# Optimization experiments

Measured on AMD Instinct MI355X. Metric: run time of the kernel, lower is better.

## Reference

```python
import jax, jax.numpy as jnp
import numpy as np

V_SRC, V_DST = 32000, 32000
E, H = 512, 512
B, S = 64, 2048


def setup_inputs() -> dict:
    key = jax.random.key(0)
    ks = jax.random.split(key, 12)
    sc = 0.02  # weight init scale
    return {
        "dec_inputs": jax.random.randint(ks[0], (1, B), 0, V_SRC, dtype=jnp.int64 if jax.config.jax_enable_x64 else jnp.int32),
        "enc_outputs": jax.random.normal(ks[1], (S, B, H), jnp.float32),
        "h0": jax.random.normal(ks[2], (1, B, H), jnp.float32),
        "emb": jax.random.normal(ks[3], (V_SRC, E), jnp.float32) * sc,
        "W_ih": jax.random.normal(ks[4], (3 * H, E), jnp.float32) * sc,
        "W_hh": jax.random.normal(ks[5], (3 * H, H), jnp.float32) * sc,
        "b_ih": jax.random.normal(ks[6], (3 * H,), jnp.float32) * sc,
        "b_hh": jax.random.normal(ks[7], (3 * H,), jnp.float32) * sc,
        "W_attn": jax.random.normal(ks[8], (H, H), jnp.float32) * sc,
        "b_attn": jax.random.normal(ks[9], (H,), jnp.float32) * sc,
        "W_cls": jax.random.normal(ks[10], (V_DST, 2 * H), jnp.float32) * sc,
        "b_cls": jax.random.normal(ks[11], (V_DST,), jnp.float32) * sc,
    }


def _gru_step(x, h, W_ih, W_hh, b_ih, b_hh):
    # x: [B, E], h: [B, H]  (PyTorch GRU gate layout: r, z, n)
    gi = x @ W_ih.T + b_ih          # [B, 3H]
    gh = h @ W_hh.T + b_hh          # [B, 3H]
    hdim = h.shape[-1]
    r = jax.nn.sigmoid(gi[:, :hdim] + gh[:, :hdim])
    z = jax.nn.sigmoid(gi[:, hdim:2 * hdim] + gh[:, hdim:2 * hdim])
    n = jnp.tanh(gi[:, 2 * hdim:] + r * gh[:, 2 * hdim:])
    return (1.0 - z) * n + z * h


def reference(dec_inputs, enc_outputs, h0, emb, W_ih, W_hh, b_ih, b_hh,
              W_attn, b_attn, W_cls, b_cls):
    # embedding + ReLU, single decode step
    x = jax.nn.relu(emb[dec_inputs[0]])                    # [B, E]
    h = _gru_step(x, h0[0], W_ih, W_hh, b_ih, b_hh)        # [B, H] == dec_output.squeeze(0)
    dec_hidden = h[None]                                   # [1, B, H]

    # attention: vectorized form of the per-timestep loop
    e = enc_outputs @ W_attn.T + b_attn                    # [S, B, H]
    alpha = jnp.einsum('sbh,bh->bs', e, h)                 # [B, S]
    scores = jax.nn.softmax(alpha, axis=1)                 # [B, S]
    context = jnp.einsum('bs,sbh->bh', scores, enc_outputs)  # [B, H]

    logits = jnp.concatenate([h, context], axis=1) @ W_cls.T + b_cls  # [B, V_dst]
    out = jax.nn.log_softmax(logits, axis=1)
    return (out, dec_hidden)
```

## Files before the change

kernel.cpp:

```cpp
#include <hip/hip_runtime.h>
#include <hip/hip_bf16.h>
#include <math.h>

#define V_SRC 32000
#define V_DST 32000
#define EDIM  512
#define HDIM  512
#define BB    64
#define SS    2048
#define G3H   1536

__global__ __launch_bounds__(128) void k_embed(const int* __restrict__ idx,
                                               const float* __restrict__ emb,
                                               float* __restrict__ x) {
    int b = blockIdx.x;
    int t = threadIdx.x;
    int row = idx[b];
    float4 v = *(const float4*)(emb + (size_t)row * EDIM + t * 4);
    v.x = fmaxf(v.x, 0.f); v.y = fmaxf(v.y, 0.f);
    v.z = fmaxf(v.z, 0.f); v.w = fmaxf(v.w, 0.f);
    *(float4*)(x + (size_t)b * EDIM + t * 4) = v;
}

__global__ __launch_bounds__(256) void k_gru_gemv(const float* __restrict__ x,
                                                  const float* __restrict__ h0,
                                                  const float* __restrict__ W_ih,
                                                  const float* __restrict__ W_hh,
                                                  float* __restrict__ gi,
                                                  float* __restrict__ gh) {
    int w    = threadIdx.x >> 6;
    int lane = threadIdx.x & 63;
    int j    = blockIdx.x * 4 + w;

    float4 wi1 = *(const float4*)(W_ih + (size_t)j * EDIM + lane * 4);
    float4 wi2 = *(const float4*)(W_ih + (size_t)j * EDIM + 256 + lane * 4);
    float4 wh1 = *(const float4*)(W_hh + (size_t)j * HDIM + lane * 4);
    float4 wh2 = *(const float4*)(W_hh + (size_t)j * HDIM + 256 + lane * 4);

    for (int b = 0; b < BB; b++) {
        float4 x1 = *(const float4*)(x  + (size_t)b * EDIM + lane * 4);
        float4 x2 = *(const float4*)(x  + (size_t)b * EDIM + 256 + lane * 4);
        float4 h1 = *(const float4*)(h0 + (size_t)b * HDIM + lane * 4);
        float4 h2 = *(const float4*)(h0 + (size_t)b * HDIM + 256 + lane * 4);
        float pi = x1.x*wi1.x + x1.y*wi1.y + x1.z*wi1.z + x1.w*wi1.w
                 + x2.x*wi2.x + x2.y*wi2.y + x2.z*wi2.z + x2.w*wi2.w;
        float ph = h1.x*wh1.x + h1.y*wh1.y + h1.z*wh1.z + h1.w*wh1.w
                 + h2.x*wh2.x + h2.y*wh2.y + h2.z*wh2.z + h2.w*wh2.w;
        #pragma unroll
        for (int off = 32; off; off >>= 1) {
            pi += __shfl_xor(pi, off);
            ph += __shfl_xor(ph, off);
        }
        if (lane == 0) {
            gi[(size_t)b * G3H + j] = pi;
            gh[(size_t)b * G3H + j] = ph;
        }
    }
}

__device__ __forceinline__ float sigmoidf_(float v) {
    return 1.f / (1.f + __expf(-v));
}

__global__ __launch_bounds__(128) void k_gru_gates(const float* __restrict__ gi,
                                                   const float* __restrict__ gh,
                                                   const float* __restrict__ h0,
                                                   const float* __restrict__ b_ih,
                                                   const float* __restrict__ b_hh,
                                                   float* __restrict__ concat,
                                                   float* __restrict__ hout) {
    int b = blockIdx.x;
    int i = threadIdx.x * 4;
    const float* gib = gi + (size_t)b * G3H;
    const float* ghb = gh + (size_t)b * G3H;

    float4 gir = *(const float4*)(gib + i);
    float4 giz = *(const float4*)(gib + i + 512);
    float4 gin = *(const float4*)(gib + i + 1024);
    float4 ghr = *(const float4*)(ghb + i);
    float4 ghz = *(const float4*)(ghb + i + 512);
    float4 ghn = *(const float4*)(ghb + i + 1024);
    float4 bir = *(const float4*)(b_ih + i);
    float4 biz = *(const float4*)(b_ih + i + 512);
    float4 bin = *(const float4*)(b_ih + i + 1024);
    float4 bhr = *(const float4*)(b_hh + i);
    float4 bhz = *(const float4*)(b_hh + i + 512);
    float4 bhn = *(const float4*)(b_hh + i + 1024);
    float4 hv  = *(const float4*)(h0 + (size_t)b * HDIM + i);

    float4 o;
    {
        float r = sigmoidf_(gir.x + bir.x + ghr.x + bhr.x);
        float z = sigmoidf_(giz.x + biz.x + ghz.x + bhz.x);
        float n = tanhf(gin.x + bin.x + r * (ghn.x + bhn.x));
        o.x = (1.f - z) * n + z * hv.x;
    }
    {
        float r = sigmoidf_(gir.y + bir.y + ghr.y + bhr.y);
        float z = sigmoidf_(giz.y + biz.y + ghz.y + bhz.y);
        float n = tanhf(gin.y + bin.y + r * (ghn.y + bhn.y));
        o.y = (1.f - z) * n + z * hv.y;
    }
    {
        float r = sigmoidf_(gir.z + bir.z + ghr.z + bhr.z);
        float z = sigmoidf_(giz.z + biz.z + ghz.z + bhz.z);
        float n = tanhf(gin.z + bin.z + r * (ghn.z + bhn.z));
        o.z = (1.f - z) * n + z * hv.z;
    }
    {
        float r = sigmoidf_(gir.w + bir.w + ghr.w + bhr.w);
        float z = sigmoidf_(giz.w + biz.w + ghz.w + bhz.w);
        float n = tanhf(gin.w + bin.w + r * (ghn.w + bhn.w));
        o.w = (1.f - z) * n + z * hv.w;
    }
    *(float4*)(concat + (size_t)b * 1024 + i) = o;
    *(float4*)(hout   + (size_t)b * HDIM + i) = o;
}

__global__ __launch_bounds__(256) void k_attn_u(const float* __restrict__ concat,
                                                const float* __restrict__ W_attn,
                                                float* __restrict__ u) {
    int b = blockIdx.x;
    int j = threadIdx.x;
    const float* hrow = concat + (size_t)b * 1024;
    float a0 = 0.f, a1 = 0.f;
    for (int i = 0; i < HDIM; i++) {
        float hvv = hrow[i];
        a0 = fmaf(hvv, W_attn[(size_t)i * HDIM + j],       a0);
        a1 = fmaf(hvv, W_attn[(size_t)i * HDIM + j + 256], a1);
    }
    u[(size_t)b * HDIM + j]       = a0;
    u[(size_t)b * HDIM + j + 256] = a1;
}

__global__ __launch_bounds__(256) void k_attn_flash(const float* __restrict__ enc,
                                                    const float* __restrict__ u,
                                                    float* __restrict__ pm,
                                                    float* __restrict__ pl,
                                                    float* __restrict__ pacc) {
    int tile = blockIdx.x;
    int b    = blockIdx.y;
    int w    = threadIdx.x >> 6;
    int lane = threadIdx.x & 63;

    float4 u1 = *(const float4*)(u + (size_t)b * HDIM + lane * 4);
    float4 u2 = *(const float4*)(u + (size_t)b * HDIM + 256 + lane * 4);

    float m = -INFINITY, l = 0.f;
    float4 a1 = {0.f, 0.f, 0.f, 0.f};
    float4 a2 = {0.f, 0.f, 0.f, 0.f};

    for (int it = 0; it < 16; it++) {
        int s = tile * 64 + it * 4 + w;
        const float* row = enc + ((size_t)s * BB + b) * HDIM;
        float4 e1 = *(const float4*)(row + lane * 4);
        float4 e2 = *(const float4*)(row + 256 + lane * 4);
        float p = e1.x*u1.x + e1.y*u1.y + e1.z*u1.z + e1.w*u1.w
                + e2.x*u2.x + e2.y*u2.y + e2.z*u2.z + e2.w*u2.w;
        #pragma unroll
        for (int off = 32; off; off >>= 1) p += __shfl_xor(p, off);

        float wt;
        if (p > m) {
            float sc = __expf(m - p);
            l *= sc;
            a1.x *= sc; a1.y *= sc; a1.z *= sc; a1.w *= sc;
            a2.x *= sc; a2.y *= sc; a2.z *= sc; a2.w *= sc;
            m = p;
            wt = 1.f;
        } else {
            wt = __expf(p - m);
        }
        l += wt;
        a1.x = fmaf(wt, e1.x, a1.x); a1.y = fmaf(wt, e1.y, a1.y);
        a1.z = fmaf(wt, e1.z, a1.z); a1.w = fmaf(wt, e1.w, a1.w);
        a2.x = fmaf(wt, e2.x, a2.x); a2.y = fmaf(wt, e2.y, a2.y);
        a2.z = fmaf(wt, e2.z, a2.z); a2.w = fmaf(wt, e2.w, a2.w);
    }

    __shared__ float sm[4], sl[4];
    __shared__ float sacc[4][512];
    if (lane == 0) { sm[w] = m; sl[w] = l; }
    *(float4*)&sacc[w][lane * 4]       = a1;
    *(float4*)&sacc[w][256 + lane * 4] = a2;
    __syncthreads();

    float M  = fmaxf(fmaxf(sm[0], sm[1]), fmaxf(sm[2], sm[3]));
    float s0 = __expf(sm[0] - M), s1 = __expf(sm[1] - M);
    float s2 = __expf(sm[2] - M), s3 = __expf(sm[3] - M);
    float L  = s0 * sl[0] + s1 * sl[1] + s2 * sl[2] + s3 * sl[3];

    int tid  = threadIdx.x;
    int pidx = b * 32 + tile;
    float acc0 = s0 * sacc[0][tid] + s1 * sacc[1][tid]
               + s2 * sacc[2][tid] + s3 * sacc[3][tid];
    float acc1 = s0 * sacc[0][tid + 256] + s1 * sacc[1][tid + 256]
               + s2 * sacc[2][tid + 256] + s3 * sacc[3][tid + 256];
    if (tid == 0) { pm[pidx] = M; pl[pidx] = L; }
    pacc[(size_t)pidx * HDIM + tid]       = acc0;
    pacc[(size_t)pidx * HDIM + tid + 256] = acc1;
}

__global__ __launch_bounds__(256) void k_attn_combine(const float* __restrict__ pm,
                                                      const float* __restrict__ pl,
                                                      const float* __restrict__ pacc,
                                                      float* __restrict__ concat) {
    int b   = blockIdx.x;
    int tid = threadIdx.x;
    __shared__ float smv[32], spl[32], ssc[32];
    if (tid < 32) {
        smv[tid] = pm[b * 32 + tid];
        spl[tid] = pl[b * 32 + tid];
    }
    __syncthreads();
    float M = smv[0];
    #pragma unroll
    for (int t = 1; t < 32; t++) M = fmaxf(M, smv[t]);
    if (tid < 32) ssc[tid] = __expf(smv[tid] - M);
    __syncthreads();

    float L = 0.f;
    #pragma unroll
    for (int t = 0; t < 32; t++) L += ssc[t] * spl[t];

    float c0 = 0.f, c1 = 0.f;
    for (int t = 0; t < 32; t++) {
        const float* pa = pacc + (size_t)(b * 32 + t) * HDIM;
        c0 = fmaf(ssc[t], pa[tid],       c0);
        c1 = fmaf(ssc[t], pa[tid + 256], c1);
    }
    float inv = 1.f / L;
    concat[(size_t)b * 1024 + 512 + tid]       = c0 * inv;
    concat[(size_t)b * 1024 + 512 + tid + 256] = c1 * inv;
}

#define LDSTR 68

__global__ __launch_bounds__(256) void k_classifier(const float* __restrict__ concat,
                                                    const float* __restrict__ W_cls,
                                                    const float* __restrict__ b_cls,
                                                    float* __restrict__ logits) {
    __shared__ float A_lds[64 * LDSTR];
    __shared__ float W_lds[64 * LDSTR];
    int t  = threadIdx.x;
    int tx = t & 15;
    int ty = t >> 4;
    int vbase = blockIdx.x * 64;
    int swz = (tx & 7) << 2;

    float acc[4][4] = {};

    for (int kc = 0; kc < 16; kc++) {
        int k0 = kc * 64;
        #pragma unroll
        for (int j = 0; j < 4; j++) {
            int idx = t + j * 256;
            int row = idx >> 4;
            int col = (idx & 15) * 4;
            float4 av = *(const float4*)(concat + (size_t)row * 1024 + k0 + col);
            *(float4*)&A_lds[row * LDSTR + col] = av;
            float4 wv = *(const float4*)(W_cls + (size_t)(vbase + row) * 1024 + k0 + col);
            int csw = col ^ (((row >> 2) & 7) << 2);
            *(float4*)&W_lds[row * LDSTR + csw] = wv;
        }
        __syncthreads();

        #pragma unroll
        for (int ks = 0; ks < 16; ks++) {
            int kk = ks * 4;
            int kw = kk ^ swz;
            float4 a0 = *(float4*)&A_lds[(ty * 4 + 0) * LDSTR + kk];
            float4 a1 = *(float4*)&A_lds[(ty * 4 + 1) * LDSTR + kk];
            float4 a2 = *(float4*)&A_lds[(ty * 4 + 2) * LDSTR + kk];
            float4 a3 = *(float4*)&A_lds[(ty * 4 + 3) * LDSTR + kk];
            float4 w0 = *(float4*)&W_lds[(tx * 4 + 0) * LDSTR + kw];
            float4 w1 = *(float4*)&W_lds[(tx * 4 + 1) * LDSTR + kw];
            float4 w2 = *(float4*)&W_lds[(tx * 4 + 2) * LDSTR + kw];
            float4 w3 = *(float4*)&W_lds[(tx * 4 + 3) * LDSTR + kw];
            float4 aa[4] = {a0, a1, a2, a3};
            float4 ww[4] = {w0, w1, w2, w3};
            #pragma unroll
            for (int i = 0; i < 4; i++)
                #pragma unroll
                for (int jj = 0; jj < 4; jj++) {
                    acc[i][jj] = fmaf(aa[i].x, ww[jj].x, acc[i][jj]);
                    acc[i][jj] = fmaf(aa[i].y, ww[jj].y, acc[i][jj]);
                    acc[i][jj] = fmaf(aa[i].z, ww[jj].z, acc[i][jj]);
                    acc[i][jj] = fmaf(aa[i].w, ww[jj].w, acc[i][jj]);
                }
        }
        __syncthreads();
    }

    float4 bc = *(const float4*)(b_cls + vbase + tx * 4);
    #pragma unroll
    for (int i = 0; i < 4; i++) {
        float4 o;
        o.x = acc[i][0] + bc.x;
        o.y = acc[i][1] + bc.y;
        o.z = acc[i][2] + bc.z;
        o.w = acc[i][3] + bc.w;
        *(float4*)&logits[(size_t)(ty * 4 + i) * V_DST + vbase + tx * 4] = o;
    }
}

__global__ __launch_bounds__(256) void k_logsoftmax(float* __restrict__ logits) {
    int b    = blockIdx.x;
    int tid  = threadIdx.x;
    int w    = tid >> 6, lane = tid & 63;
    float4* row = (float4*)(logits + (size_t)b * V_DST);
    __shared__ float sm4[4], sl4[4];

    float m = -INFINITY;
    for (int i = tid; i < 8000; i += 256) {
        float4 v = row[i];
        m = fmaxf(m, fmaxf(fmaxf(v.x, v.y), fmaxf(v.z, v.w)));
    }
    #pragma unroll
    for (int off = 32; off; off >>= 1) m = fmaxf(m, __shfl_xor(m, off));
    if (lane == 0) sm4[w] = m;
    __syncthreads();
    float M = fmaxf(fmaxf(sm4[0], sm4[1]), fmaxf(sm4[2], sm4[3]));

    float l = 0.f;
    for (int i = tid; i < 8000; i += 256) {
        float4 v = row[i];
        l += __expf(v.x - M) + __expf(v.y - M) + __expf(v.z - M) + __expf(v.w - M);
    }
    #pragma unroll
    for (int off = 32; off; off >>= 1) l += __shfl_xor(l, off);
    if (lane == 0) sl4[w] = l;
    __syncthreads();
    float L   = sl4[0] + sl4[1] + sl4[2] + sl4[3];
    float lse = M + logf(L);

    for (int i = tid; i < 8000; i += 256) {
        float4 v = row[i];
        v.x -= lse; v.y -= lse; v.z -= lse; v.w -= lse;
        row[i] = v;
    }
}

extern "C" void kernel_launch(void* const* d_in, const int* in_sizes, int n_in,
                              void* d_out, int out_size, void* d_ws, size_t ws_size,
                              hipStream_t stream) {
    const int*   dec_inputs = (const int*)  d_in[0];
    const float* enc        = (const float*)d_in[1];
    const float* h0         = (const float*)d_in[2];
    const float* emb        = (const float*)d_in[3];
    const float* W_ih       = (const float*)d_in[4];
    const float* W_hh       = (const float*)d_in[5];
    const float* b_ih       = (const float*)d_in[6];
    const float* b_hh       = (const float*)d_in[7];
    const float* W_attn     = (const float*)d_in[8];
    const float* W_cls      = (const float*)d_in[10];
    const float* b_cls      = (const float*)d_in[11];

    float* out  = (float*)d_out;
    float* hout = out + (size_t)BB * V_DST;

    float* ws     = (float*)d_ws;
    float* x      = ws;
    float* gi     = ws + 32768;
    float* gh     = ws + 131072;
    float* concat = ws + 229376;
    float* u      = ws + 294912;
    float* pm     = ws + 327680;
    float* pl     = ws + 329728;
    float* pacc   = ws + 331776;

    k_embed      <<<64,          128, 0, stream>>>(dec_inputs, emb, x);
    k_gru_gemv   <<<384,         256, 0, stream>>>(x, h0, W_ih, W_hh, gi, gh);
    k_gru_gates  <<<64,          128, 0, stream>>>(gi, gh, h0, b_ih, b_hh, concat, hout);
    k_attn_u     <<<64,          256, 0, stream>>>(concat, W_attn, u);
    k_attn_flash <<<dim3(32,64), 256, 0, stream>>>(enc, u, pm, pl, pacc);
    k_attn_combine<<<64,         256, 0, stream>>>(pm, pl, pacc, concat);
    k_classifier <<<500,         256, 0, stream>>>(concat, W_cls, b_cls, out);
    k_logsoftmax <<<64,          256, 0, stream>>>(out);
}
```

Before: 641.7 us.

## Use split-bf16 MFMA classifier, fuse embed into GRU, split attention projection, partial log-softmax

The classifier GEMM now runs on bf16 MFMA instructions. Activations are pre-split into high and low bf16 halves and weights are split on the fly, with three MFMA products per step to approximate fp32 accuracy. The classifier also emits per-block max and sum partials, so the log-softmax kernel only needs one read-modify-write pass instead of three passes over the logits. The embedding gather with ReLU is fused into the GRU GEMV, and the attention projection is split over K chunks for more parallelism. The three-term bf16 split may lose some precision compared with fp32 FMA.

```diff
diff --git a/kernel.cpp b/kernel.cpp
--- a/kernel.cpp
+++ b/kernel.cpp
@@ -10,19 +10,25 @@
 #define SS    2048
 #define G3H   1536
 
-__global__ __launch_bounds__(128) void k_embed(const int* __restrict__ idx,
-                                               const float* __restrict__ emb,
-                                               float* __restrict__ x) {
-    int b = blockIdx.x;
-    int t = threadIdx.x;
-    int row = idx[b];
-    float4 v = *(const float4*)(emb + (size_t)row * EDIM + t * 4);
-    v.x = fmaxf(v.x, 0.f); v.y = fmaxf(v.y, 0.f);
-    v.z = fmaxf(v.z, 0.f); v.w = fmaxf(v.w, 0.f);
-    *(float4*)(x + (size_t)b * EDIM + t * 4) = v;
-}
-
-__global__ __launch_bounds__(256) void k_gru_gemv(const float* __restrict__ x,
+typedef __attribute__((ext_vector_type(8))) short bfrag8;
+typedef __attribute__((ext_vector_type(4))) float f4v;
+
+__device__ __forceinline__ void split_bf16(float x, unsigned short& h, unsigned short& l) {
+    unsigned u  = __float_as_uint(x);
+    unsigned hb = u & 0xFFFF0000u;
+    h = (unsigned short)(u >> 16);
+    float r = x - __uint_as_float(hb);
+    unsigned v = __float_as_uint(r);
+    v += 0x7FFFu + ((v >> 16) & 1u);
+    l = (unsigned short)(v >> 16);
+}
+
+__device__ __forceinline__ float sigmoidf_(float v) {
+    return 1.f / (1.f + __expf(-v));
+}
+
+__global__ __launch_bounds__(256) void k_gru_gemv(const int* __restrict__ idx,
+                                                  const float* __restrict__ emb,
                                                   const float* __restrict__ h0,
                                                   const float* __restrict__ W_ih,
                                                   const float* __restrict__ W_hh,
@@ -38,8 +44,14 @@
     float4 wh2 = *(const float4*)(W_hh + (size_t)j * HDIM + 256 + lane * 4);
 
     for (int b = 0; b < BB; b++) {
-        float4 x1 = *(const float4*)(x  + (size_t)b * EDIM + lane * 4);
-        float4 x2 = *(const float4*)(x  + (size_t)b * EDIM + 256 + lane * 4);
+        int row = idx[b];
+        const float* er = emb + (size_t)row * EDIM;
+        float4 x1 = *(const float4*)(er + lane * 4);
+        float4 x2 = *(const float4*)(er + 256 + lane * 4);
+        x1.x = fmaxf(x1.x, 0.f); x1.y = fmaxf(x1.y, 0.f);
+        x1.z = fmaxf(x1.z, 0.f); x1.w = fmaxf(x1.w, 0.f);
+        x2.x = fmaxf(x2.x, 0.f); x2.y = fmaxf(x2.y, 0.f);
+        x2.z = fmaxf(x2.z, 0.f); x2.w = fmaxf(x2.w, 0.f);
         float4 h1 = *(const float4*)(h0 + (size_t)b * HDIM + lane * 4);
         float4 h2 = *(const float4*)(h0 + (size_t)b * HDIM + 256 + lane * 4);
         float pi = x1.x*wi1.x + x1.y*wi1.y + x1.z*wi1.z + x1.w*wi1.w
@@ -58,17 +70,15 @@
     }
 }
 
-__device__ __forceinline__ float sigmoidf_(float v) {
-    return 1.f / (1.f + __expf(-v));
-}
-
 __global__ __launch_bounds__(128) void k_gru_gates(const float* __restrict__ gi,
                                                    const float* __restrict__ gh,
                                                    const float* __restrict__ h0,
                                                    const float* __restrict__ b_ih,
                                                    const float* __restrict__ b_hh,
-                                                   float* __restrict__ concat,
-                                                   float* __restrict__ hout) {
+                                                   float* __restrict__ h,
+                                                   float* __restrict__ hout,
+                                                   unsigned short* __restrict__ cH,
+                                                   unsigned short* __restrict__ cL) {
     int b = blockIdx.x;
     int i = threadIdx.x * 4;
     const float* gib = gi + (size_t)b * G3H;
@@ -88,53 +98,55 @@
     float4 bhn = *(const float4*)(b_hh + i + 1024);
     float4 hv  = *(const float4*)(h0 + (size_t)b * HDIM + i);
 
-    float4 o;
-    {
-        float r = sigmoidf_(gir.x + bir.x + ghr.x + bhr.x);
-        float z = sigmoidf_(giz.x + biz.x + ghz.x + bhz.x);
-        float n = tanhf(gin.x + bin.x + r * (ghn.x + bhn.x));
-        o.x = (1.f - z) * n + z * hv.x;
-    }
-    {
-        float r = sigmoidf_(gir.y + bir.y + ghr.y + bhr.y);
-        float z = sigmoidf_(giz.y + biz.y + ghz.y + bhz.y);
-        float n = tanhf(gin.y + bin.y + r * (ghn.y + bhn.y));
-        o.y = (1.f - z) * n + z * hv.y;
-    }
-    {
-        float r = sigmoidf_(gir.z + bir.z + ghr.z + bhr.z);
-        float z = sigmoidf_(giz.z + biz.z + ghz.z + bhz.z);
-        float n = tanhf(gin.z + bin.z + r * (ghn.z + bhn.z));
-        o.z = (1.f - z) * n + z * hv.z;
-    }
-    {
-        float r = sigmoidf_(gir.w + bir.w + ghr.w + bhr.w);
-        float z = sigmoidf_(giz.w + biz.w + ghz.w + bhz.w);
-        float n = tanhf(gin.w + bin.w + r * (ghn.w + bhn.w));
-        o.w = (1.f - z) * n + z * hv.w;
-    }
-    *(float4*)(concat + (size_t)b * 1024 + i) = o;
-    *(float4*)(hout   + (size_t)b * HDIM + i) = o;
-}
-
-__global__ __launch_bounds__(256) void k_attn_u(const float* __restrict__ concat,
-                                                const float* __restrict__ W_attn,
-                                                float* __restrict__ u) {
-    int b = blockIdx.x;
-    int j = threadIdx.x;
-    const float* hrow = concat + (size_t)b * 1024;
+    float o[4], hvv[4] = {hv.x, hv.y, hv.z, hv.w};
+    float girv[4] = {gir.x, gir.y, gir.z, gir.w}, gizv[4] = {giz.x, giz.y, giz.z, giz.w};
+    float ginv[4] = {gin.x, gin.y, gin.z, gin.w}, ghrv[4] = {ghr.x, ghr.y, ghr.z, ghr.w};
+    float ghzv[4] = {ghz.x, ghz.y, ghz.z, ghz.w}, ghnv[4] = {ghn.x, ghn.y, ghn.z, ghn.w};
+    float birv[4] = {bir.x, bir.y, bir.z, bir.w}, bizv[4] = {biz.x, biz.y, biz.z, biz.w};
+    float binv[4] = {bin.x, bin.y, bin.z, bin.w}, bhrv[4] = {bhr.x, bhr.y, bhr.z, bhr.w};
+    float bhzv[4] = {bhz.x, bhz.y, bhz.z, bhz.w}, bhnv[4] = {bhn.x, bhn.y, bhn.z, bhn.w};
+
+    unsigned short hs[4], ls[4];
+    #pragma unroll
+    for (int q = 0; q < 4; q++) {
+        float r = sigmoidf_(girv[q] + birv[q] + ghrv[q] + bhrv[q]);
+        float z = sigmoidf_(gizv[q] + bizv[q] + ghzv[q] + bhzv[q]);
+        float n = tanhf(ginv[q] + binv[q] + r * (ghnv[q] + bhnv[q]));
+        o[q] = (1.f - z) * n + z * hvv[q];
+        split_bf16(o[q], hs[q], ls[q]);
+    }
+    float4 of = {o[0], o[1], o[2], o[3]};
+    *(float4*)(h    + (size_t)b * HDIM + i) = of;
+    *(float4*)(hout + (size_t)b * HDIM + i) = of;
+    ushort4 hh = {hs[0], hs[1], hs[2], hs[3]};
+    ushort4 ll = {ls[0], ls[1], ls[2], ls[3]};
+    *(ushort4*)(cH + (size_t)b * 1024 + i) = hh;
+    *(ushort4*)(cL + (size_t)b * 1024 + i) = ll;
+}
+
+__global__ __launch_bounds__(256) void k_u(const float* __restrict__ h,
+                                           const float* __restrict__ W_attn,
+                                           float* __restrict__ u_part) {
+    int kc = blockIdx.x;
+    int b  = blockIdx.y;
+    int t  = threadIdx.x;
+    __shared__ float hl[64];
+    if (t < 64) hl[t] = h[(size_t)b * HDIM + kc * 64 + t];
+    __syncthreads();
+    const float* Wp = W_attn + (size_t)(kc * 64) * HDIM;
     float a0 = 0.f, a1 = 0.f;
-    for (int i = 0; i < HDIM; i++) {
-        float hvv = hrow[i];
-        a0 = fmaf(hvv, W_attn[(size_t)i * HDIM + j],       a0);
-        a1 = fmaf(hvv, W_attn[(size_t)i * HDIM + j + 256], a1);
-    }
-    u[(size_t)b * HDIM + j]       = a0;
-    u[(size_t)b * HDIM + j + 256] = a1;
+    #pragma unroll 8
+    for (int i = 0; i < 64; i++) {
+        float hv = hl[i];
+        a0 = fmaf(hv, Wp[(size_t)i * HDIM + t],       a0);
+        a1 = fmaf(hv, Wp[(size_t)i * HDIM + t + 256], a1);
+    }
+    u_part[(size_t)(kc * 64 + b) * HDIM + t]       = a0;
+    u_part[(size_t)(kc * 64 + b) * HDIM + t + 256] = a1;
 }
 
 __global__ __launch_bounds__(256) void k_attn_flash(const float* __restrict__ enc,
-                                                    const float* __restrict__ u,
+                                                    const float* __restrict__ u_part,
                                                     float* __restrict__ pm,
                                                     float* __restrict__ pl,
                                                     float* __restrict__ pacc) {
@@ -143,8 +155,15 @@
     int w    = threadIdx.x >> 6;
     int lane = threadIdx.x & 63;
 
-    float4 u1 = *(const float4*)(u + (size_t)b * HDIM + lane * 4);
-    float4 u2 = *(const float4*)(u + (size_t)b * HDIM + 256 + lane * 4);
+    float4 u1 = {0.f,0.f,0.f,0.f}, u2 = {0.f,0.f,0.f,0.f};
+    #pragma unroll
+    for (int kc = 0; kc < 8; kc++) {
+        const float* up = u_part + (size_t)(kc * 64 + b) * HDIM;
+        float4 p1 = *(const float4*)(up + lane * 4);
+        float4 p2 = *(const float4*)(up + 256 + lane * 4);
+        u1.x += p1.x; u1.y += p1.y; u1.z += p1.z; u1.w += p1.w;
+        u2.x += p2.x; u2.y += p2.y; u2.z += p2.z; u2.w += p2.w;
+    }
 
     float m = -INFINITY, l = 0.f;
     float4 a1 = {0.f, 0.f, 0.f, 0.f};
@@ -204,7 +223,8 @@
 __global__ __launch_bounds__(256) void k_attn_combine(const float* __restrict__ pm,
                                                       const float* __restrict__ pl,
                                                       const float* __restrict__ pacc,
-                                                      float* __restrict__ concat) {
+                                                      unsigned short* __restrict__ cH,
+                                                      unsigned short* __restrict__ cL) {
     int b   = blockIdx.x;
     int tid = threadIdx.x;
     __shared__ float smv[32], spl[32], ssc[32];
@@ -230,111 +250,128 @@
         c1 = fmaf(ssc[t], pa[tid + 256], c1);
     }
     float inv = 1.f / L;
-    concat[(size_t)b * 1024 + 512 + tid]       = c0 * inv;
-    concat[(size_t)b * 1024 + 512 + tid + 256] = c1 * inv;
-}
-
-#define LDSTR 68
-
-__global__ __launch_bounds__(256) void k_classifier(const float* __restrict__ concat,
+    c0 *= inv; c1 *= inv;
+    unsigned short h0s, l0s, h1s, l1s;
+    split_bf16(c0, h0s, l0s);
+    split_bf16(c1, h1s, l1s);
+    cH[(size_t)b * 1024 + 512 + tid]       = h0s;
+    cL[(size_t)b * 1024 + 512 + tid]       = l0s;
+    cH[(size_t)b * 1024 + 512 + tid + 256] = h1s;
+    cL[(size_t)b * 1024 + 512 + tid + 256] = l1s;
+}
+
+__global__ __launch_bounds__(512) void k_classifier(const unsigned short* __restrict__ cH,
+                                                    const unsigned short* __restrict__ cL,
                                                     const float* __restrict__ W_cls,
                                                     const float* __restrict__ b_cls,
-                                                    float* __restrict__ logits) {
-    __shared__ float A_lds[64 * LDSTR];
-    __shared__ float W_lds[64 * LDSTR];
-    int t  = threadIdx.x;
-    int tx = t & 15;
-    int ty = t >> 4;
-    int vbase = blockIdx.x * 64;
-    int swz = (tx & 7) << 2;
-
-    float acc[4][4] = {};
-
-    for (int kc = 0; kc < 16; kc++) {
-        int k0 = kc * 64;
-        #pragma unroll
-        for (int j = 0; j < 4; j++) {
-            int idx = t + j * 256;
-            int row = idx >> 4;
-            int col = (idx & 15) * 4;
-            float4 av = *(const float4*)(concat + (size_t)row * 1024 + k0 + col);
-            *(float4*)&A_lds[row * LDSTR + col] = av;
-            float4 wv = *(const float4*)(W_cls + (size_t)(vbase + row) * 1024 + k0 + col);
-            int csw = col ^ (((row >> 2) & 7) << 2);
-            *(float4*)&W_lds[row * LDSTR + csw] = wv;
-        }
-        __syncthreads();
-
-        #pragma unroll
-        for (int ks = 0; ks < 16; ks++) {
-            int kk = ks * 4;
-            int kw = kk ^ swz;
-            float4 a0 = *(float4*)&A_lds[(ty * 4 + 0) * LDSTR + kk];
-            float4 a1 = *(float4*)&A_lds[(ty * 4 + 1) * LDSTR + kk];
-            float4 a2 = *(float4*)&A_lds[(ty * 4 + 2) * LDSTR + kk];
-            float4 a3 = *(float4*)&A_lds[(ty * 4 + 3) * LDSTR + kk];
-            float4 w0 = *(float4*)&W_lds[(tx * 4 + 0) * LDSTR + kw];
-            float4 w1 = *(float4*)&W_lds[(tx * 4 + 1) * LDSTR + kw];
-            float4 w2 = *(float4*)&W_lds[(tx * 4 + 2) * LDSTR + kw];
-            float4 w3 = *(float4*)&W_lds[(tx * 4 + 3) * LDSTR + kw];
-            float4 aa[4] = {a0, a1, a2, a3};
-            float4 ww[4] = {w0, w1, w2, w3};
-            #pragma unroll
-            for (int i = 0; i < 4; i++)
-                #pragma unroll
-                for (int jj = 0; jj < 4; jj++) {
-                    acc[i][jj] = fmaf(aa[i].x, ww[jj].x, acc[i][jj]);
-                    acc[i][jj] = fmaf(aa[i].y, ww[jj].y, acc[i][jj]);
-                    acc[i][jj] = fmaf(aa[i].z, ww[jj].z, acc[i][jj]);
-                    acc[i][jj] = fmaf(aa[i].w, ww[jj].w, acc[i][jj]);
-                }
-        }
-        __syncthreads();
-    }
-
-    float4 bc = *(const float4*)(b_cls + vbase + tx * 4);
-    #pragma unroll
-    for (int i = 0; i < 4; i++) {
-        float4 o;
-        o.x = acc[i][0] + bc.x;
-        o.y = acc[i][1] + bc.y;
-        o.z = acc[i][2] + bc.z;
-        o.w = acc[i][3] + bc.w;
-        *(float4*)&logits[(size_t)(ty * 4 + i) * V_DST + vbase + tx * 4] = o;
-    }
-}
-
-__global__ __launch_bounds__(256) void k_logsoftmax(float* __restrict__ logits) {
-    int b    = blockIdx.x;
-    int tid  = threadIdx.x;
-    int w    = tid >> 6, lane = tid & 63;
-    float4* row = (float4*)(logits + (size_t)b * V_DST);
+                                                    float* __restrict__ logits,
+                                                    float* __restrict__ pmax,
+                                                    float* __restrict__ psum) {
+    int t = threadIdx.x;
+    int w = t >> 6;
+    int l = t & 63;
+    int g = l >> 4;
+    int bl = l & 15;
+    int v_lane = blockIdx.x * 128 + w * 16 + bl;
+
+    const float* pW = W_cls + (size_t)v_lane * 1024 + g * 8;
+    const unsigned short* pAh[4];
+    const unsigned short* pAl[4];
+    #pragma unroll
+    for (int bq = 0; bq < 4; bq++) {
+        pAh[bq] = cH + (size_t)(bq * 16 + bl) * 1024 + g * 8;
+        pAl[bq] = cL + (size_t)(bq * 16 + bl) * 1024 + g * 8;
+    }
+
+    f4v acc[4] = {};
+
+    #pragma unroll 2
+    for (int k0 = 0; k0 < 1024; k0 += 32) {
+        float4 wf0 = *(const float4*)(pW + k0);
+        float4 wf1 = *(const float4*)(pW + k0 + 4);
+        float wf[8] = {wf0.x, wf0.y, wf0.z, wf0.w, wf1.x, wf1.y, wf1.z, wf1.w};
+        bfrag8 wh, wl;
+        #pragma unroll
+        for (int q = 0; q < 8; q++) {
+            unsigned short hs, ls;
+            split_bf16(wf[q], hs, ls);
+            wh[q] = (short)hs;
+            wl[q] = (short)ls;
+        }
+        #pragma unroll
+        for (int bq = 0; bq < 4; bq++) {
+            bfrag8 ah = *(const bfrag8*)(pAh[bq] + k0);
+            bfrag8 al = *(const bfrag8*)(pAl[bq] + k0);
+            acc[bq] = __builtin_amdgcn_mfma_f32_16x16x32_bf16(ah, wh, acc[bq], 0, 0, 0);
+            acc[bq] = __builtin_amdgcn_mfma_f32_16x16x32_bf16(al, wh, acc[bq], 0, 0, 0);
+            acc[bq] = __builtin_amdgcn_mfma_f32_16x16x32_bf16(ah, wl, acc[bq], 0, 0, 0);
+        }
+    }
+
+    float bias = b_cls[v_lane];
+
+    #pragma unroll
+    for (int bq = 0; bq < 4; bq++) {
+        #pragma unroll
+        for (int r = 0; r < 4; r++) {
+            float val = acc[bq][r] + bias;
+            int brow = bq * 16 + g * 4 + r;
+            logits[(size_t)brow * V_DST + v_lane] = val;
+        }
+    }
+    size_t pbase = ((size_t)blockIdx.x * 8 + w) * 64;
+    #pragma unroll
+    for (int bq = 0; bq < 4; bq++) {
+        #pragma unroll
+        for (int r = 0; r < 4; r++) {
+            float val = acc[bq][r] + bias;
+            float mv = val;
+            mv = fmaxf(mv, __shfl_xor(mv, 1));
+            mv = fmaxf(mv, __shfl_xor(mv, 2));
+            mv = fmaxf(mv, __shfl_xor(mv, 4));
+            mv = fmaxf(mv, __shfl_xor(mv, 8));
+            float e = __expf(val - mv);
+            e += __shfl_xor(e, 1);
+            e += __shfl_xor(e, 2);
+            e += __shfl_xor(e, 4);
+            e += __shfl_xor(e, 8);
+            if (bl == 0) {
+                int brow = bq * 16 + g * 4 + r;
+                pmax[pbase + brow] = mv;
+                psum[pbase + brow] = e;
+            }
+        }
+    }
+}
+
+__global__ __launch_bounds__(256) void k_lsm(const float* __restrict__ pmax,
+                                             const float* __restrict__ psum,
+                                             float* __restrict__ logits) {
+    int c = blockIdx.x;
+    int b = blockIdx.y;
+    int tid = threadIdx.x;
+    int w = tid >> 6, lane = tid & 63;
     __shared__ float sm4[4], sl4[4];
 
     float m = -INFINITY;
-    for (int i = tid; i < 8000; i += 256) {
-        float4 v = row[i];
-        m = fmaxf(m, fmaxf(fmaxf(v.x, v.y), fmaxf(v.z, v.w)));
-    }
+    for (int i = tid; i < 2000; i += 256) m = fmaxf(m, pmax[(size_t)i * 64 + b]);
     #pragma unroll
     for (int off = 32; off; off >>= 1) m = fmaxf(m, __shfl_xor(m, off));
     if (lane == 0) sm4[w] = m;
     __syncthreads();
     float M = fmaxf(fmaxf(sm4[0], sm4[1]), fmaxf(sm4[2], sm4[3]));
 
-    float l = 0.f;
-    for (int i = tid; i < 8000; i += 256) {
-        float4 v = row[i];
-        l += __expf(v.x - M) + __expf(v.y - M) + __expf(v.z - M) + __expf(v.w - M);
-    }
-    #pragma unroll
-    for (int off = 32; off; off >>= 1) l += __shfl_xor(l, off);
-    if (lane == 0) sl4[w] = l;
-    __syncthreads();
-    float L   = sl4[0] + sl4[1] + sl4[2] + sl4[3];
-    float lse = M + logf(L);
-
-    for (int i = tid; i < 8000; i += 256) {
+    float s = 0.f;
+    for (int i = tid; i < 2000; i += 256)
+        s += psum[(size_t)i * 64 + b] * __expf(pmax[(size_t)i * 64 + b] - M);
+    #pragma unroll
+    for (int off = 32; off; off >>= 1) s += __shfl_xor(s, off);
+    if (lane == 0) sl4[w] = s;
+    __syncthreads();
+    float lse = M + logf(sl4[0] + sl4[1] + sl4[2] + sl4[3]);
+
+    float4* row = (float4*)(logits + (size_t)b * V_DST) + c * 2000;
+    for (int i = tid; i < 2000; i += 256) {
         float4 v = row[i];
         v.x -= lse; v.y -= lse; v.z -= lse; v.w -= lse;
         row[i] = v;
@@ -359,22 +396,24 @@
     float* out  = (float*)d_out;
     float* hout = out + (size_t)BB * V_DST;
 
-    float* ws     = (float*)d_ws;
-    float* x      = ws;
-    float* gi     = ws + 32768;
-    float* gh     = ws + 131072;
-    float* concat = ws + 229376;
-    float* u      = ws + 294912;
-    float* pm     = ws + 327680;
-    float* pl     = ws + 329728;
-    float* pacc   = ws + 331776;
-
-    k_embed      <<<64,          128, 0, stream>>>(dec_inputs, emb, x);
-    k_gru_gemv   <<<384,         256, 0, stream>>>(x, h0, W_ih, W_hh, gi, gh);
-    k_gru_gates  <<<64,          128, 0, stream>>>(gi, gh, h0, b_ih, b_hh, concat, hout);
-    k_attn_u     <<<64,          256, 0, stream>>>(concat, W_attn, u);
-    k_attn_flash <<<dim3(32,64), 256, 0, stream>>>(enc, u, pm, pl, pacc);
-    k_attn_combine<<<64,         256, 0, stream>>>(pm, pl, pacc, concat);
-    k_classifier <<<500,         256, 0, stream>>>(concat, W_cls, b_cls, out);
-    k_logsoftmax <<<64,          256, 0, stream>>>(out);
-}
+    char* ws = (char*)d_ws;
+    float*          gi     = (float*)(ws + 0);
+    float*          gh     = (float*)(ws + 393216);
+    float*          h      = (float*)(ws + 786432);
+    float*          u_part = (float*)(ws + 917504);
+    float*          pm     = (float*)(ws + 1966080);
+    float*          pl     = (float*)(ws + 1974272);
+    float*          pacc   = (float*)(ws + 1982464);
+    unsigned short* cH     = (unsigned short*)(ws + 6176768);
+    unsigned short* cL     = (unsigned short*)(ws + 6307840);
+    float*          pmax   = (float*)(ws + 6438912);
+    float*          psum   = (float*)(ws + 6950912);
+
+    k_gru_gemv    <<<384,          256, 0, stream>>>(dec_inputs, emb, h0, W_ih, W_hh, gi, gh);
+    k_gru_gates   <<<64,           128, 0, stream>>>(gi, gh, h0, b_ih, b_hh, h, hout, cH, cL);
+    k_u           <<<dim3(8, 64),  256, 0, stream>>>(h, W_attn, u_part);
+    k_attn_flash  <<<dim3(32, 64), 256, 0, stream>>>(enc, u_part, pm, pl, pacc);
+    k_attn_combine<<<64,           256, 0, stream>>>(pm, pl, pacc, cH, cL);
+    k_classifier  <<<250,          512, 0, stream>>>(cH, cL, W_cls, b_cls, out, pmax, psum);
+    k_lsm         <<<dim3(4, 64),  256, 0, stream>>>(pmax, psum, out);
+}
```

New measurement: 628.9 us. 2.0% less time.
